# Optimization experiments

Hardware: AMD Instinct MI355X
Metric: run time of the kernel (lower is better)

## Reference

```python
import jax, jax.numpy as jnp
import numpy as np

D = 64          # node/edge feature dim
DIN = 3 * D     # concat [src, edge, dst]
N_NODES = 30000
N_EDGES = 480000


def _lin_init(key, fan_in, fan_out):
    return jax.random.normal(key, (fan_in, fan_out), dtype=jnp.float32) / np.sqrt(fan_in)


def setup_inputs() -> dict:
    key = jax.random.key(0)
    ks = jax.random.split(key, 24)
    inp = {
        "node_feat": jax.random.normal(ks[0], (N_NODES, D), dtype=jnp.float32),
        "edge_feat": jax.random.normal(ks[1], (N_EDGES, D), dtype=jnp.float32),
        "src": jax.random.randint(ks[2], (N_EDGES,), 0, N_NODES, dtype=jnp.int32),
        "dst": jax.random.randint(ks[3], (N_EDGES,), 0, N_NODES, dtype=jnp.int32),
    }
    # GatedMLP params for edge update and node update: each has a 'layers' MLP
    # [192->64->64] (SiLU after both layers) and a 'gates' MLP [192->64->64]
    # (SiLU after hidden only, then sigmoid).
    i = 4
    for pref in ("edge", "node"):
        for branch in ("layers", "gates"):
            inp[f"{pref}_{branch}_W0"] = _lin_init(ks[i], DIN, D); i += 1
            inp[f"{pref}_{branch}_b0"] = jnp.zeros((D,), jnp.float32)
            inp[f"{pref}_{branch}_W1"] = _lin_init(ks[i], D, D); i += 1
            inp[f"{pref}_{branch}_b1"] = jnp.zeros((D,), jnp.float32)
    inp["node_out_W"] = _lin_init(ks[i], D, D)  # Linear(64,64,bias=False)
    return inp


def _gated_mlp(x, lW0, lb0, lW1, lb1, gW0, gb0, gW1, gb1):
    silu = jax.nn.silu
    # layers branch: activate hidden + last
    h = silu(silu(x @ lW0 + lb0) @ lW1 + lb1)
    # gates branch: activate hidden only, sigmoid at the end
    g = silu(x @ gW0 + gb0) @ gW1 + gb1
    return h * jax.nn.sigmoid(g)


def reference(node_feat, edge_feat, src, dst,
              edge_layers_W0, edge_layers_b0, edge_layers_W1, edge_layers_b1,
              edge_gates_W0, edge_gates_b0, edge_gates_W1, edge_gates_b1,
              node_layers_W0, node_layers_b0, node_layers_W1, node_layers_b1,
              node_gates_W0, node_gates_b0, node_gates_W1, node_gates_b1,
              node_out_W):
    h_src = node_feat[src]            # [E, D] gather
    h_dst = node_feat[dst]            # [E, D] gather
    # edge update: gated MLP on [src || edge || dst], residual
    e_in = jnp.concatenate([h_src, edge_feat, h_dst], axis=-1)  # [E, 3D]
    e_new = edge_feat + _gated_mlp(e_in, edge_layers_W0, edge_layers_b0,
                                   edge_layers_W1, edge_layers_b1,
                                   edge_gates_W0, edge_gates_b0,
                                   edge_gates_W1, edge_gates_b1)
    # node messages: gated MLP on [src || new_edge || dst]
    m_in = jnp.concatenate([h_src, e_new, h_dst], axis=-1)      # [E, 3D]
    msg = _gated_mlp(m_in, node_layers_W0, node_layers_b0,
                     node_layers_W1, node_layers_b1,
                     node_gates_W0, node_gates_b0,
                     node_gates_W1, node_gates_b1)
    # scatter-sum to destination nodes, output linear, residual
    agg = jax.ops.segment_sum(msg, dst, num_segments=node_feat.shape[0])
    h_new = node_feat + agg @ node_out_W
    return h_new, e_new
```

## Files before the change

### kernel.cpp

```cpp
#include <hip/hip_runtime.h>
#include <hip/hip_bf16.h>
#include <math.h>

typedef __bf16 bf16_t;
typedef __bf16 bf16x8 __attribute__((ext_vector_type(8)));
typedef float  f32x4  __attribute__((ext_vector_type(4)));

#define MFMA16(a,b,c) __builtin_amdgcn_mfma_f32_16x16x32_bf16((a),(b),(c),0,0,0)

namespace {
constexpr int D    = 64;
constexpr int DIN  = 192;
constexpr int NN   = 30000;
constexpr int NE   = 480000;
constexpr int TILE = 128;
constexpr int NTILES = NE / TILE;

constexpr int SW0 = 200;
constexpr int SW1 = 72;
constexpr int SH  = 72;

constexpr int W0T_SZ = 64 * SW0;
constexpr int W1T_SZ = 64 * SW1;

constexpr int LDS_A = 0;
constexpr int LDS_B = 12800;
constexpr int LDS_C = 22016;
constexpr int LDS_TOT = 31232;

constexpr size_t WS_AGG_BYTES = (size_t)NN * D * 4;
constexpr size_t WS_WT_BYTES  = (size_t)(4 * W0T_SZ + 4 * W1T_SZ) * 2;
constexpr size_t WS_FLAG_OFF  = WS_AGG_BYTES + WS_WT_BYTES;
}

__device__ __forceinline__ bf16x8 ldA(const bf16_t* p) {
  return *(const bf16x8*)p;
}
__device__ __forceinline__ bf16x8 ldA(const float* p) {
  const float4* q4 = (const float4*)p;
  const float4 u = q4[0], v = q4[1];
  bf16x8 r;
  r[0] = (bf16_t)u.x; r[1] = (bf16_t)u.y; r[2] = (bf16_t)u.z; r[3] = (bf16_t)u.w;
  r[4] = (bf16_t)v.x; r[5] = (bf16_t)v.y; r[6] = (bf16_t)v.z; r[7] = (bf16_t)v.w;
  return r;
}

__device__ __forceinline__ void stage16(bf16_t* l, const bf16_t* g, int elems, int t) {
  int4* ls = (int4*)l; const int4* gs = (const int4*)g;
  const int n = elems >> 3;
  for (int i = t; i < n; i += 256) ls[i] = gs[i];
}

__device__ __forceinline__ float silu_f(float v) { return v / (1.f + __expf(-v)); }
__device__ __forceinline__ float sigm_f(float v) { return 1.f / (1.f + __expf(-v)); }

template<typename TN, typename TM>
__device__ __forceinline__ void mlp_l0(f32x4 acc[2][4], const bf16_t* __restrict__ w0t,
    const TN* __restrict__ nf, const TM* __restrict__ mid,
    int sA, int sB, int dA, int dB, int midA, int midB, int midStride,
    int m, int q)
{
  const f32x4 z = {0.f, 0.f, 0.f, 0.f};
  #pragma unroll
  for (int mt = 0; mt < 2; ++mt)
    #pragma unroll
    for (int nt = 0; nt < 4; ++nt) acc[mt][nt] = z;
  #pragma unroll
  for (int kt = 0; kt < 6; ++kt) {
    const int ko = (kt & 1) * 32 + q * 8;
    bf16x8 a0, a1;
    if (kt < 2)      { a0 = ldA(nf + sA * D + ko);            a1 = ldA(nf + sB * D + ko); }
    else if (kt < 4) { a0 = ldA(mid + midA * midStride + ko); a1 = ldA(mid + midB * midStride + ko); }
    else             { a0 = ldA(nf + dA * D + ko);            a1 = ldA(nf + dB * D + ko); }
    const bf16_t* wb = w0t + m * SW0 + kt * 32 + q * 8;
    #pragma unroll
    for (int nt = 0; nt < 4; ++nt) {
      const bf16x8 b = ldA(wb + nt * 16 * SW0);
      acc[0][nt] = MFMA16(a0, b, acc[0][nt]);
      acc[1][nt] = MFMA16(a1, b, acc[1][nt]);
    }
  }
}

__device__ __forceinline__ void mlp_l1(f32x4 acc[2][4], const bf16_t* __restrict__ h,
                                       const bf16_t* __restrict__ w1t,
                                       int leA, int leB, int m, int q)
{
  const f32x4 z = {0.f, 0.f, 0.f, 0.f};
  #pragma unroll
  for (int mt = 0; mt < 2; ++mt)
    #pragma unroll
    for (int nt = 0; nt < 4; ++nt) acc[mt][nt] = z;
  #pragma unroll
  for (int kt = 0; kt < 2; ++kt) {
    const int ko = kt * 32 + q * 8;
    const bf16x8 a0 = ldA(h + leA * SH + ko);
    const bf16x8 a1 = ldA(h + leB * SH + ko);
    const bf16_t* wb = w1t + m * SW1 + ko;
    #pragma unroll
    for (int nt = 0; nt < 4; ++nt) {
      const bf16x8 b = ldA(wb + nt * 16 * SW1);
      acc[0][nt] = MFMA16(a0, b, acc[0][nt]);
      acc[1][nt] = MFMA16(a1, b, acc[1][nt]);
    }
  }
}

template<typename TB>
__device__ __forceinline__ void hidden_silu(const f32x4 acc[2][4],
    const TB* __restrict__ bias, bf16_t* __restrict__ h, int w, int m, int q)
{
  #pragma unroll
  for (int nt = 0; nt < 4; ++nt) {
    const float bv = (float)bias[nt * 16 + m];
    #pragma unroll
    for (int mt = 0; mt < 2; ++mt) {
      #pragma unroll
      for (int r = 0; r < 4; ++r) {
        const float v = acc[mt][nt][r] + bv;
        h[(w * 32 + mt * 16 + q * 4 + r) * SH + nt * 16 + m] = (bf16_t)silu_f(v);
      }
    }
  }
}

__global__ void detect_kernel(const void* w0, int* flag) {
  __shared__ int cnt;
  if (threadIdx.x == 0) cnt = 0;
  __syncthreads();
  const unsigned short* u = (const unsigned short*)w0;
  const unsigned short v = u[2 * threadIdx.x];
  const int e = (v >> 7) & 0xFF;
  atomicAdd(&cnt, (e >= 100 && e <= 140) ? 1 : 0);
  __syncthreads();
  if (threadIdx.x == 0) *flag = (cnt >= 128) ? 1 : 0;
}

struct PrepArgs { const void* w[8]; bf16_t* o[8]; };

template<typename T>
__global__ void prep_kernel(const int* flag, int want, PrepArgs a) {
  if (*flag != want) return;
  const int b = blockIdx.x, t = threadIdx.x;
  const T* w = (const T*)a.w[b];
  bf16_t* o = a.o[b];
  if (b < 4) {
    for (int i = t; i < DIN * D; i += 256) o[(i & 63) * SW0 + (i >> 6)] = (bf16_t)(float)w[i];
  } else {
    for (int i = t; i < D * D; i += 256) o[(i & 63) * SW1 + (i >> 6)] = (bf16_t)(float)w[i];
  }
}

template<typename T>
__global__ __launch_bounds__(256, 2) void fused_kernel(
    const int* __restrict__ flag, int want,
    const T* __restrict__ nf, const T* __restrict__ ef,
    const int* __restrict__ src, const int* __restrict__ dst,
    const T* __restrict__ eLb0, const T* __restrict__ eLb1,
    const T* __restrict__ eGb0, const T* __restrict__ eGb1,
    const T* __restrict__ nLb0, const T* __restrict__ nLb1,
    const T* __restrict__ nGb0, const T* __restrict__ nGb1,
    const bf16_t* __restrict__ wt, float* __restrict__ agg,
    T* __restrict__ out_e)
{
  if (*flag != want) return;
  __shared__ __align__(16) bf16_t sm[LDS_TOT];
  const int t = threadIdx.x;
  const int lane = t & 63;
  const int w = t >> 6;
  const int m = lane & 15;
  const int q = lane >> 4;

  const bf16_t* w0t_eL = wt;
  const bf16_t* w0t_eG = wt + W0T_SZ;
  const bf16_t* w0t_nL = wt + 2 * W0T_SZ;
  const bf16_t* w0t_nG = wt + 3 * W0T_SZ;
  const bf16_t* w1t_e  = wt + 4 * W0T_SZ;
  const bf16_t* w1t_n  = wt + 4 * W0T_SZ + 2 * W1T_SZ;

  for (int tile = blockIdx.x; tile < NTILES; tile += gridDim.x) {
    const int e0  = tile * TILE;
    const int eA  = e0 + w * 32 + m;
    const int eB  = eA + 16;
    const int leA = w * 32 + m;
    const int leB = leA + 16;
    const int sA = src[eA], sB = src[eB];
    const int dA = dst[eA], dB = dst[eB];

    f32x4 acc[2][4], acg[2][4];

    stage16(sm + LDS_A, w0t_eL, W0T_SZ, t);
    __syncthreads();
    mlp_l0(acc, sm + LDS_A, nf, ef, sA, sB, dA, dB, eA, eB, D, m, q);
    hidden_silu(acc, eLb0, sm + LDS_B, w, m, q);
    __syncthreads();
    stage16(sm + LDS_A, w0t_eG, W0T_SZ, t);
    __syncthreads();
    mlp_l0(acc, sm + LDS_A, nf, ef, sA, sB, dA, dB, eA, eB, D, m, q);
    hidden_silu(acc, eGb0, sm + LDS_C, w, m, q);
    __syncthreads();
    stage16(sm + LDS_A, w1t_e, 2 * W1T_SZ, t);
    __syncthreads();
    mlp_l1(acc, sm + LDS_B, sm + LDS_A,          leA, leB, m, q);
    mlp_l1(acg, sm + LDS_C, sm + LDS_A + W1T_SZ, leA, leB, m, q);

    bf16_t ev[2][4][4];
    #pragma unroll
    for (int nt = 0; nt < 4; ++nt) {
      const int n = nt * 16 + m;
      const float bL = (float)eLb1[n];
      const float bG = (float)eGb1[n];
      #pragma unroll
      for (int mt = 0; mt < 2; ++mt) {
        #pragma unroll
        for (int r = 0; r < 4; ++r) {
          const int e = e0 + w * 32 + mt * 16 + q * 4 + r;
          const float hv = silu_f(acc[mt][nt][r] + bL);
          const float gv = sigm_f(acg[mt][nt][r] + bG);
          const float val = (float)ef[e * D + n] + hv * gv;
          ev[mt][nt][r] = (bf16_t)val;
          out_e[e * D + n] = (T)val;
        }
      }
    }
    __syncthreads();
    #pragma unroll
    for (int nt = 0; nt < 4; ++nt)
      #pragma unroll
      for (int mt = 0; mt < 2; ++mt)
        #pragma unroll
        for (int r = 0; r < 4; ++r)
          sm[LDS_B + (w * 32 + mt * 16 + q * 4 + r) * SH + nt * 16 + m] = ev[mt][nt][r];
    __syncthreads();

    stage16(sm + LDS_A, w0t_nL, W0T_SZ, t);
    __syncthreads();
    mlp_l0(acc, sm + LDS_A, nf, sm + LDS_B, sA, sB, dA, dB, leA, leB, SH, m, q);
    hidden_silu(acc, nLb0, sm + LDS_C, w, m, q);
    __syncthreads();
    stage16(sm + LDS_A, w0t_nG, W0T_SZ, t);
    __syncthreads();
    mlp_l0(acc, sm + LDS_A, nf, sm + LDS_B, sA, sB, dA, dB, leA, leB, SH, m, q);
    __syncthreads();
    hidden_silu(acc, nGb0, sm + LDS_B, w, m, q);
    __syncthreads();
    stage16(sm + LDS_A, w1t_n, 2 * W1T_SZ, t);
    __syncthreads();
    mlp_l1(acc, sm + LDS_C, sm + LDS_A,          leA, leB, m, q);
    mlp_l1(acg, sm + LDS_B, sm + LDS_A + W1T_SZ, leA, leB, m, q);

    int d8[2][4];
    #pragma unroll
    for (int mt = 0; mt < 2; ++mt)
      #pragma unroll
      for (int r = 0; r < 4; ++r)
        d8[mt][r] = dst[e0 + w * 32 + mt * 16 + q * 4 + r];

    #pragma unroll
    for (int nt = 0; nt < 4; ++nt) {
      const int n = nt * 16 + m;
      const float bL = (float)nLb1[n];
      const float bG = (float)nGb1[n];
      #pragma unroll
      for (int mt = 0; mt < 2; ++mt) {
        #pragma unroll
        for (int r = 0; r < 4; ++r) {
          const float hv = silu_f(acc[mt][nt][r] + bL);
          const float gv = sigm_f(acg[mt][nt][r] + bG);
          atomicAdd(&agg[d8[mt][r] * D + n], hv * gv);
        }
      }
    }
    __syncthreads();
  }
}

template<typename T>
__global__ __launch_bounds__(256) void node_out_kernel(
    const int* __restrict__ flag, int want,
    const T* __restrict__ nf, const float* __restrict__ agg,
    const T* __restrict__ Wo, T* __restrict__ out_h)
{
  if (*flag != want) return;
  __shared__ float wsh[D * D];
  const int t = threadIdx.x;
  for (int i = t; i < D * D; i += 256) wsh[i] = (float)Wo[i];
  __syncthreads();
  const int node = blockIdx.x * 4 + (t >> 6);
  const int j = t & 63;
  const float* arow = agg + node * D;
  float acc = 0.f;
  #pragma unroll
  for (int k = 0; k < D; ++k) acc = fmaf(arow[k], wsh[k * D + j], acc);
  out_h[node * D + j] = (T)((float)nf[node * D + j] + acc);
}

template<typename T>
static void launch_all(void* const* d_in, void* d_out, void* d_ws,
                       const int* flag, int want, bf16_t* wt, float* agg,
                       hipStream_t stream) {
  const T* nf  = (const T*)d_in[0];
  const T* ef  = (const T*)d_in[1];
  const int* src = (const int*)d_in[2];
  const int* dst = (const int*)d_in[3];
  T* out_h = (T*)d_out;
  T* out_e = out_h + (size_t)NN * D;

  fused_kernel<T><<<512, 256, 0, stream>>>(flag, want, nf, ef, src, dst,
      (const T*)d_in[5],  (const T*)d_in[7],
      (const T*)d_in[9],  (const T*)d_in[11],
      (const T*)d_in[13], (const T*)d_in[15],
      (const T*)d_in[17], (const T*)d_in[19],
      wt, agg, out_e);
  node_out_kernel<T><<<NN / 4, 256, 0, stream>>>(flag, want, nf, agg,
      (const T*)d_in[20], out_h);
}

extern "C" void kernel_launch(void* const* d_in, const int* in_sizes, int n_in,
                              void* d_out, int out_size, void* d_ws, size_t ws_size,
                              hipStream_t stream) {
  float*  agg  = (float*)d_ws;
  bf16_t* wt   = (bf16_t*)((char*)d_ws + WS_AGG_BYTES);
  int*    flag = (int*)((char*)d_ws + WS_FLAG_OFF);

  hipMemsetAsync(d_ws, 0, WS_AGG_BYTES, stream);

  detect_kernel<<<1, 256, 0, stream>>>(d_in[4], flag);

  PrepArgs pa;
  pa.w[0] = d_in[4];  pa.w[1] = d_in[8];  pa.w[2] = d_in[12]; pa.w[3] = d_in[16];
  pa.w[4] = d_in[6];  pa.w[5] = d_in[10]; pa.w[6] = d_in[14]; pa.w[7] = d_in[18];
  for (int i = 0; i < 4; ++i) pa.o[i]     = wt + i * W0T_SZ;
  for (int j = 0; j < 4; ++j) pa.o[4 + j] = wt + 4 * W0T_SZ + j * W1T_SZ;
  prep_kernel<float> <<<8, 256, 0, stream>>>(flag, 0, pa);
  prep_kernel<bf16_t><<<8, 256, 0, stream>>>(flag, 1, pa);

  launch_all<float> (d_in, d_out, d_ws, flag, 0, wt, agg, stream);
  launch_all<bf16_t>(d_in, d_out, d_ws, flag, 1, wt, agg, stream);
}
```

Before: 613.2 us.

## Make each wave own a 32-edge chunk, reading weights from global memory without block syncs

The block-wide tile loop, with its repeated LDS weight staging and many __syncthreads, is replaced by per-wave 32-edge chunks that read the transposed bf16 weights straight from global memory (L1/L2-cached). Hidden activations use per-wave LDS slots. The layers and gates first-layer GEMMs are fused into one pass that shares the A-operand loads. Node features are pre-converted to bf16 in a separate kernel, and the grid grows with launch bounds raised to 4 blocks per SM. The trade is more global/L1 weight traffic per wave and an extra conversion kernel, in exchange for removing barriers and staging.

```diff
diff --git a/kernel.cpp b/kernel.cpp
--- a/kernel.cpp
+++ b/kernel.cpp
@@ -9,33 +9,28 @@
 #define MFMA16(a,b,c) __builtin_amdgcn_mfma_f32_16x16x32_bf16((a),(b),(c),0,0,0)
 
 namespace {
-constexpr int D    = 64;
-constexpr int DIN  = 192;
-constexpr int NN   = 30000;
-constexpr int NE   = 480000;
-constexpr int TILE = 128;
-constexpr int NTILES = NE / TILE;
-
-constexpr int SW0 = 200;
-constexpr int SW1 = 72;
+constexpr int D   = 64;
+constexpr int DIN = 192;
+constexpr int NN  = 30000;
+constexpr int NE  = 480000;
+constexpr int NCH = NE / 32;
+constexpr int GRID = 1250;
 constexpr int SH  = 72;
-
-constexpr int W0T_SZ = 64 * SW0;
-constexpr int W1T_SZ = 64 * SW1;
-
-constexpr int LDS_A = 0;
-constexpr int LDS_B = 12800;
-constexpr int LDS_C = 22016;
-constexpr int LDS_TOT = 31232;
-
-constexpr size_t WS_AGG_BYTES = (size_t)NN * D * 4;
-constexpr size_t WS_WT_BYTES  = (size_t)(4 * W0T_SZ + 4 * W1T_SZ) * 2;
-constexpr size_t WS_FLAG_OFF  = WS_AGG_BYTES + WS_WT_BYTES;
-}
-
-__device__ __forceinline__ bf16x8 ldA(const bf16_t* p) {
-  return *(const bf16x8*)p;
-}
+constexpr int SLOT = 32 * SH;
+
+constexpr int W0_SZ = 64 * 192;
+constexpr int W1_SZ = 64 * 64;
+
+constexpr size_t WS_AGG   = 0;
+constexpr size_t AGG_B    = (size_t)NN * D * 4;
+constexpr size_t WS_WT    = AGG_B;
+constexpr size_t WT_B     = (size_t)(4 * W0_SZ + 4 * W1_SZ) * 2;
+constexpr size_t WS_NF    = WS_WT + WT_B;
+constexpr size_t NF_B     = (size_t)NN * D * 2;
+constexpr size_t WS_FLAG  = WS_NF + NF_B;
+}
+
+__device__ __forceinline__ bf16x8 ldA(const bf16_t* p) { return *(const bf16x8*)p; }
 __device__ __forceinline__ bf16x8 ldA(const float* p) {
   const float4* q4 = (const float4*)p;
   const float4 u = q4[0], v = q4[1];
@@ -45,18 +40,13 @@
   return r;
 }
 
-__device__ __forceinline__ void stage16(bf16_t* l, const bf16_t* g, int elems, int t) {
-  int4* ls = (int4*)l; const int4* gs = (const int4*)g;
-  const int n = elems >> 3;
-  for (int i = t; i < n; i += 256) ls[i] = gs[i];
-}
-
 __device__ __forceinline__ float silu_f(float v) { return v / (1.f + __expf(-v)); }
 __device__ __forceinline__ float sigm_f(float v) { return 1.f / (1.f + __expf(-v)); }
 
-template<typename TN, typename TM>
-__device__ __forceinline__ void mlp_l0(f32x4 acc[2][4], const bf16_t* __restrict__ w0t,
-    const TN* __restrict__ nf, const TM* __restrict__ mid,
+template<typename TM>
+__device__ __forceinline__ void mlp_l0_pair(f32x4 acc[2][4], f32x4 acg[2][4],
+    const bf16_t* __restrict__ wL, const bf16_t* __restrict__ wG,
+    const bf16_t* __restrict__ nfb, const TM* __restrict__ mid,
     int sA, int sB, int dA, int dB, int midA, int midB, int midStride,
     int m, int q)
 {
@@ -64,63 +54,64 @@
   #pragma unroll
   for (int mt = 0; mt < 2; ++mt)
     #pragma unroll
-    for (int nt = 0; nt < 4; ++nt) acc[mt][nt] = z;
+    for (int nt = 0; nt < 4; ++nt) { acc[mt][nt] = z; acg[mt][nt] = z; }
   #pragma unroll
   for (int kt = 0; kt < 6; ++kt) {
     const int ko = (kt & 1) * 32 + q * 8;
     bf16x8 a0, a1;
-    if (kt < 2)      { a0 = ldA(nf + sA * D + ko);            a1 = ldA(nf + sB * D + ko); }
+    if (kt < 2)      { a0 = ldA(nfb + sA * D + ko);           a1 = ldA(nfb + sB * D + ko); }
     else if (kt < 4) { a0 = ldA(mid + midA * midStride + ko); a1 = ldA(mid + midB * midStride + ko); }
-    else             { a0 = ldA(nf + dA * D + ko);            a1 = ldA(nf + dB * D + ko); }
-    const bf16_t* wb = w0t + m * SW0 + kt * 32 + q * 8;
+    else             { a0 = ldA(nfb + dA * D + ko);           a1 = ldA(nfb + dB * D + ko); }
+    const bf16_t* bl = wL + m * 192 + kt * 32 + q * 8;
+    const bf16_t* bg = wG + m * 192 + kt * 32 + q * 8;
     #pragma unroll
     for (int nt = 0; nt < 4; ++nt) {
-      const bf16x8 b = ldA(wb + nt * 16 * SW0);
+      const bf16x8 bL8 = ldA(bl + nt * 16 * 192);
+      acc[0][nt] = MFMA16(a0, bL8, acc[0][nt]);
+      acc[1][nt] = MFMA16(a1, bL8, acc[1][nt]);
+      const bf16x8 bG8 = ldA(bg + nt * 16 * 192);
+      acg[0][nt] = MFMA16(a0, bG8, acg[0][nt]);
+      acg[1][nt] = MFMA16(a1, bG8, acg[1][nt]);
+    }
+  }
+}
+
+__device__ __forceinline__ void mlp_l1(f32x4 acc[2][4], const bf16_t* __restrict__ h,
+                                       const bf16_t* __restrict__ w1t, int m, int q)
+{
+  const f32x4 z = {0.f, 0.f, 0.f, 0.f};
+  #pragma unroll
+  for (int mt = 0; mt < 2; ++mt)
+    #pragma unroll
+    for (int nt = 0; nt < 4; ++nt) acc[mt][nt] = z;
+  #pragma unroll
+  for (int kt = 0; kt < 2; ++kt) {
+    const int ko = kt * 32 + q * 8;
+    const bf16x8 a0 = ldA(h + m * SH + ko);
+    const bf16x8 a1 = ldA(h + (m + 16) * SH + ko);
+    const bf16_t* wb = w1t + m * 64 + ko;
+    #pragma unroll
+    for (int nt = 0; nt < 4; ++nt) {
+      const bf16x8 b = ldA(wb + nt * 16 * 64);
       acc[0][nt] = MFMA16(a0, b, acc[0][nt]);
       acc[1][nt] = MFMA16(a1, b, acc[1][nt]);
     }
   }
 }
 
-__device__ __forceinline__ void mlp_l1(f32x4 acc[2][4], const bf16_t* __restrict__ h,
-                                       const bf16_t* __restrict__ w1t,
-                                       int leA, int leB, int m, int q)
-{
-  const f32x4 z = {0.f, 0.f, 0.f, 0.f};
-  #pragma unroll
-  for (int mt = 0; mt < 2; ++mt)
-    #pragma unroll
-    for (int nt = 0; nt < 4; ++nt) acc[mt][nt] = z;
-  #pragma unroll
-  for (int kt = 0; kt < 2; ++kt) {
-    const int ko = kt * 32 + q * 8;
-    const bf16x8 a0 = ldA(h + leA * SH + ko);
-    const bf16x8 a1 = ldA(h + leB * SH + ko);
-    const bf16_t* wb = w1t + m * SW1 + ko;
-    #pragma unroll
-    for (int nt = 0; nt < 4; ++nt) {
-      const bf16x8 b = ldA(wb + nt * 16 * SW1);
-      acc[0][nt] = MFMA16(a0, b, acc[0][nt]);
-      acc[1][nt] = MFMA16(a1, b, acc[1][nt]);
-    }
-  }
-}
-
 template<typename TB>
 __device__ __forceinline__ void hidden_silu(const f32x4 acc[2][4],
-    const TB* __restrict__ bias, bf16_t* __restrict__ h, int w, int m, int q)
+    const TB* __restrict__ bias, bf16_t* __restrict__ h, int m, int q)
 {
   #pragma unroll
   for (int nt = 0; nt < 4; ++nt) {
     const float bv = (float)bias[nt * 16 + m];
     #pragma unroll
-    for (int mt = 0; mt < 2; ++mt) {
+    for (int mt = 0; mt < 2; ++mt)
       #pragma unroll
-      for (int r = 0; r < 4; ++r) {
-        const float v = acc[mt][nt][r] + bv;
-        h[(w * 32 + mt * 16 + q * 4 + r) * SH + nt * 16 + m] = (bf16_t)silu_f(v);
-      }
-    }
+      for (int r = 0; r < 4; ++r)
+        h[(mt * 16 + q * 4 + r) * SH + nt * 16 + m] =
+            (bf16_t)silu_f(acc[mt][nt][r] + bv);
   }
 }
 
@@ -139,22 +130,31 @@
 struct PrepArgs { const void* w[8]; bf16_t* o[8]; };
 
 template<typename T>
-__global__ void prep_kernel(const int* flag, int want, PrepArgs a) {
+__global__ void prep_w_kernel(const int* flag, int want, PrepArgs a) {
   if (*flag != want) return;
   const int b = blockIdx.x, t = threadIdx.x;
   const T* w = (const T*)a.w[b];
   bf16_t* o = a.o[b];
   if (b < 4) {
-    for (int i = t; i < DIN * D; i += 256) o[(i & 63) * SW0 + (i >> 6)] = (bf16_t)(float)w[i];
+    for (int i = t; i < DIN * D; i += 256) o[(i & 63) * 192 + (i >> 6)] = (bf16_t)(float)w[i];
   } else {
-    for (int i = t; i < D * D; i += 256) o[(i & 63) * SW1 + (i >> 6)] = (bf16_t)(float)w[i];
-  }
-}
-
-template<typename T>
-__global__ __launch_bounds__(256, 2) void fused_kernel(
+    for (int i = t; i < D * D; i += 256)  o[(i & 63) * 64  + (i >> 6)] = (bf16_t)(float)w[i];
+  }
+}
+
+template<typename T>
+__global__ void prep_nf_kernel(const int* flag, int want,
+                               const T* __restrict__ nf, bf16_t* __restrict__ nfb) {
+  if (*flag != want) return;
+  const int n8 = NN * D / 8;
+  for (int i = blockIdx.x * 256 + threadIdx.x; i < n8; i += gridDim.x * 256)
+    *(bf16x8*)(nfb + i * 8) = ldA(nf + i * 8);
+}
+
+template<typename T>
+__global__ __launch_bounds__(256, 4) void fused_kernel(
     const int* __restrict__ flag, int want,
-    const T* __restrict__ nf, const T* __restrict__ ef,
+    const bf16_t* __restrict__ nfb, const T* __restrict__ ef,
     const int* __restrict__ src, const int* __restrict__ dst,
     const T* __restrict__ eLb0, const T* __restrict__ eLb1,
     const T* __restrict__ eGb0, const T* __restrict__ eGb1,
@@ -164,97 +164,70 @@
     T* __restrict__ out_e)
 {
   if (*flag != want) return;
-  __shared__ __align__(16) bf16_t sm[LDS_TOT];
+  __shared__ __align__(16) bf16_t sm[4 * 2 * SLOT];
   const int t = threadIdx.x;
   const int lane = t & 63;
   const int w = t >> 6;
   const int m = lane & 15;
   const int q = lane >> 4;
 
-  const bf16_t* w0t_eL = wt;
-  const bf16_t* w0t_eG = wt + W0T_SZ;
-  const bf16_t* w0t_nL = wt + 2 * W0T_SZ;
-  const bf16_t* w0t_nG = wt + 3 * W0T_SZ;
-  const bf16_t* w1t_e  = wt + 4 * W0T_SZ;
-  const bf16_t* w1t_n  = wt + 4 * W0T_SZ + 2 * W1T_SZ;
-
-  for (int tile = blockIdx.x; tile < NTILES; tile += gridDim.x) {
-    const int e0  = tile * TILE;
-    const int eA  = e0 + w * 32 + m;
-    const int eB  = eA + 16;
-    const int leA = w * 32 + m;
-    const int leB = leA + 16;
+  bf16_t* hB = sm + w * (2 * SLOT);
+  bf16_t* hC = hB + SLOT;
+
+  const bf16_t* w0eL = wt;
+  const bf16_t* w0eG = wt + W0_SZ;
+  const bf16_t* w0nL = wt + 2 * W0_SZ;
+  const bf16_t* w0nG = wt + 3 * W0_SZ;
+  const bf16_t* w1eL = wt + 4 * W0_SZ;
+  const bf16_t* w1eG = wt + 4 * W0_SZ + W1_SZ;
+  const bf16_t* w1nL = wt + 4 * W0_SZ + 2 * W1_SZ;
+  const bf16_t* w1nG = wt + 4 * W0_SZ + 3 * W1_SZ;
+
+  const int wid = blockIdx.x * 4 + w;
+  for (int c = wid; c < NCH; c += GRID * 4) {
+    const int e0 = c * 32;
+    const int eA = e0 + m, eB = eA + 16;
     const int sA = src[eA], sB = src[eB];
     const int dA = dst[eA], dB = dst[eB];
 
     f32x4 acc[2][4], acg[2][4];
 
-    stage16(sm + LDS_A, w0t_eL, W0T_SZ, t);
-    __syncthreads();
-    mlp_l0(acc, sm + LDS_A, nf, ef, sA, sB, dA, dB, eA, eB, D, m, q);
-    hidden_silu(acc, eLb0, sm + LDS_B, w, m, q);
-    __syncthreads();
-    stage16(sm + LDS_A, w0t_eG, W0T_SZ, t);
-    __syncthreads();
-    mlp_l0(acc, sm + LDS_A, nf, ef, sA, sB, dA, dB, eA, eB, D, m, q);
-    hidden_silu(acc, eGb0, sm + LDS_C, w, m, q);
-    __syncthreads();
-    stage16(sm + LDS_A, w1t_e, 2 * W1T_SZ, t);
-    __syncthreads();
-    mlp_l1(acc, sm + LDS_B, sm + LDS_A,          leA, leB, m, q);
-    mlp_l1(acg, sm + LDS_C, sm + LDS_A + W1T_SZ, leA, leB, m, q);
-
-    bf16_t ev[2][4][4];
+    mlp_l0_pair(acc, acg, w0eL, w0eG, nfb, ef, sA, sB, dA, dB, eA, eB, D, m, q);
+    hidden_silu(acc, eLb0, hB, m, q);
+    hidden_silu(acg, eGb0, hC, m, q);
+    mlp_l1(acc, hB, w1eL, m, q);
+    mlp_l1(acg, hC, w1eG, m, q);
+
     #pragma unroll
     for (int nt = 0; nt < 4; ++nt) {
       const int n = nt * 16 + m;
       const float bL = (float)eLb1[n];
       const float bG = (float)eGb1[n];
       #pragma unroll
-      for (int mt = 0; mt < 2; ++mt) {
+      for (int mt = 0; mt < 2; ++mt)
         #pragma unroll
         for (int r = 0; r < 4; ++r) {
-          const int e = e0 + w * 32 + mt * 16 + q * 4 + r;
+          const int e = e0 + mt * 16 + q * 4 + r;
           const float hv = silu_f(acc[mt][nt][r] + bL);
           const float gv = sigm_f(acg[mt][nt][r] + bG);
           const float val = (float)ef[e * D + n] + hv * gv;
-          ev[mt][nt][r] = (bf16_t)val;
           out_e[e * D + n] = (T)val;
+          hB[(mt * 16 + q * 4 + r) * SH + n] = (bf16_t)val;
         }
-      }
     }
-    __syncthreads();
-    #pragma unroll
-    for (int nt = 0; nt < 4; ++nt)
-      #pragma unroll
-      for (int mt = 0; mt < 2; ++mt)
-        #pragma unroll
-        for (int r = 0; r < 4; ++r)
-          sm[LDS_B + (w * 32 + mt * 16 + q * 4 + r) * SH + nt * 16 + m] = ev[mt][nt][r];
-    __syncthreads();
-
-    stage16(sm + LDS_A, w0t_nL, W0T_SZ, t);
-    __syncthreads();
-    mlp_l0(acc, sm + LDS_A, nf, sm + LDS_B, sA, sB, dA, dB, leA, leB, SH, m, q);
-    hidden_silu(acc, nLb0, sm + LDS_C, w, m, q);
-    __syncthreads();
-    stage16(sm + LDS_A, w0t_nG, W0T_SZ, t);
-    __syncthreads();
-    mlp_l0(acc, sm + LDS_A, nf, sm + LDS_B, sA, sB, dA, dB, leA, leB, SH, m, q);
-    __syncthreads();
-    hidden_silu(acc, nGb0, sm + LDS_B, w, m, q);
-    __syncthreads();
-    stage16(sm + LDS_A, w1t_n, 2 * W1T_SZ, t);
-    __syncthreads();
-    mlp_l1(acc, sm + LDS_C, sm + LDS_A,          leA, leB, m, q);
-    mlp_l1(acg, sm + LDS_B, sm + LDS_A + W1T_SZ, leA, leB, m, q);
+
+    mlp_l0_pair(acc, acg, w0nL, w0nG, nfb, hB, sA, sB, dA, dB, m, m + 16, SH, m, q);
+    hidden_silu(acc, nLb0, hC, m, q);
+    hidden_silu(acg, nGb0, hB, m, q);
+    mlp_l1(acc, hC, w1nL, m, q);
+    mlp_l1(acg, hB, w1nG, m, q);
 
     int d8[2][4];
     #pragma unroll
     for (int mt = 0; mt < 2; ++mt)
       #pragma unroll
       for (int r = 0; r < 4; ++r)
-        d8[mt][r] = dst[e0 + w * 32 + mt * 16 + q * 4 + r];
+        d8[mt][r] = dst[e0 + mt * 16 + q * 4 + r];
 
     #pragma unroll
     for (int nt = 0; nt < 4; ++nt) {
@@ -262,16 +235,14 @@
       const float bL = (float)nLb1[n];
       const float bG = (float)nGb1[n];
       #pragma unroll
-      for (int mt = 0; mt < 2; ++mt) {
+      for (int mt = 0; mt < 2; ++mt)
         #pragma unroll
         for (int r = 0; r < 4; ++r) {
           const float hv = silu_f(acc[mt][nt][r] + bL);
           const float gv = sigm_f(acg[mt][nt][r] + bG);
           atomicAdd(&agg[d8[mt][r] * D + n], hv * gv);
         }
-      }
     }
-    __syncthreads();
   }
 }
 
@@ -296,9 +267,9 @@
 }
 
 template<typename T>
-static void launch_all(void* const* d_in, void* d_out, void* d_ws,
-                       const int* flag, int want, bf16_t* wt, float* agg,
-                       hipStream_t stream) {
+static void launch_all(void* const* d_in, void* d_out,
+                       const int* flag, int want, const bf16_t* wt,
+                       const bf16_t* nfb, float* agg, hipStream_t stream) {
   const T* nf  = (const T*)d_in[0];
   const T* ef  = (const T*)d_in[1];
   const int* src = (const int*)d_in[2];
@@ -306,7 +277,8 @@
   T* out_h = (T*)d_out;
   T* out_e = out_h + (size_t)NN * D;
 
-  fused_kernel<T><<<512, 256, 0, stream>>>(flag, want, nf, ef, src, dst,
+  prep_nf_kernel<T><<<512, 256, 0, stream>>>(flag, want, nf, (bf16_t*)nfb);
+  fused_kernel<T><<<GRID, 256, 0, stream>>>(flag, want, nfb, ef, src, dst,
       (const T*)d_in[5],  (const T*)d_in[7],
       (const T*)d_in[9],  (const T*)d_in[11],
       (const T*)d_in[13], (const T*)d_in[15],
@@ -320,21 +292,22 @@
                               void* d_out, int out_size, void* d_ws, size_t ws_size,
                               hipStream_t stream) {
   float*  agg  = (float*)d_ws;
-  bf16_t* wt   = (bf16_t*)((char*)d_ws + WS_AGG_BYTES);
-  int*    flag = (int*)((char*)d_ws + WS_FLAG_OFF);
-
-  hipMemsetAsync(d_ws, 0, WS_AGG_BYTES, stream);
+  bf16_t* wt   = (bf16_t*)((char*)d_ws + WS_WT);
+  bf16_t* nfb  = (bf16_t*)((char*)d_ws + WS_NF);
+  int*    flag = (int*)((char*)d_ws + WS_FLAG);
+
+  hipMemsetAsync(d_ws, 0, AGG_B, stream);
 
   detect_kernel<<<1, 256, 0, stream>>>(d_in[4], flag);
 
   PrepArgs pa;
   pa.w[0] = d_in[4];  pa.w[1] = d_in[8];  pa.w[2] = d_in[12]; pa.w[3] = d_in[16];
   pa.w[4] = d_in[6];  pa.w[5] = d_in[10]; pa.w[6] = d_in[14]; pa.w[7] = d_in[18];
-  for (int i = 0; i < 4; ++i) pa.o[i]     = wt + i * W0T_SZ;
-  for (int j = 0; j < 4; ++j) pa.o[4 + j] = wt + 4 * W0T_SZ + j * W1T_SZ;
-  prep_kernel<float> <<<8, 256, 0, stream>>>(flag, 0, pa);
-  prep_kernel<bf16_t><<<8, 256, 0, stream>>>(flag, 1, pa);
-
-  launch_all<float> (d_in, d_out, d_ws, flag, 0, wt, agg, stream);
-  launch_all<bf16_t>(d_in, d_out, d_ws, flag, 1, wt, agg, stream);
-}
+  for (int i = 0; i < 4; ++i) pa.o[i]     = wt + i * W0_SZ;
+  for (int j = 0; j < 4; ++j) pa.o[4 + j] = wt + 4 * W0_SZ + j * W1_SZ;
+  prep_w_kernel<float> <<<8, 256, 0, stream>>>(flag, 0, pa);
+  prep_w_kernel<bf16_t><<<8, 256, 0, stream>>>(flag, 1, pa);
+
+  launch_all<float> (d_in, d_out, flag, 0, wt, nfb, agg, stream);
+  launch_all<bf16_t>(d_in, d_out, flag, 1, wt, nfb, agg, stream);
+}
```

Result: slower. 1.175 ms (+91.6%).
